# Optimization experiments

Hardware: AMD Instinct MI355X
Metric: run time of the kernel (lower is better)

## Reference

```python
import jax, jax.numpy as jnp
import numpy as np

EPS = 1e-8
LN_EPS = 1e-5
CAPACITY_BETA = 1.5
IDEAL_CLASSES = 5.0

B, F, E, H, C, G = 8192, 1024, 30, 256, 100, 4096


def setup_inputs() -> dict:
    key = jax.random.key(0)
    ks = jax.random.split(key, 8)
    x = jax.random.normal(ks[0], (B, F), dtype=jnp.float32)
    prototypes = jax.random.normal(ks[1], (E, F), dtype=jnp.float32)
    g_new = jax.random.normal(ks[2], (G,), dtype=jnp.float32)
    g_mem = jax.random.normal(ks[3], (E, G), dtype=jnp.float32)
    class_counts = jax.random.randint(ks[4], (E,), 0, 12, dtype=jnp.int32)
    W1 = jax.random.normal(ks[5], (E, F, H), dtype=jnp.float32) * (1.0 / np.sqrt(F))
    b1 = jnp.zeros((E, H), dtype=jnp.float32)
    gamma = jnp.ones((E, H), dtype=jnp.float32)
    beta = jnp.zeros((E, H), dtype=jnp.float32)
    W2 = jax.random.normal(ks[6], (E, H, C), dtype=jnp.float32) * (1.0 / np.sqrt(H))
    b2 = jnp.zeros((E, C), dtype=jnp.float32)
    return {"x": x, "prototypes": prototypes, "g_new": g_new, "g_mem": g_mem,
            "class_counts": class_counts, "W1": W1, "b1": b1, "gamma": gamma,
            "beta": beta, "W2": W2, "b2": b2}


def _route_scores(x, prototypes, g_new, g_mem, class_counts):
    # Cosine similarity of each sample to each expert prototype: [B, E]
    xn = x / (jnp.linalg.norm(x, axis=-1, keepdims=True) + EPS)
    pn = prototypes / (jnp.linalg.norm(prototypes, axis=-1, keepdims=True) + EPS)
    sim = xn @ pn.T
    # Gradient alignment score per expert (cosine of new grad vs EMA memory), mapped to [0, 1]
    gn = g_new / (jnp.linalg.norm(g_new) + EPS)
    gm = g_mem / (jnp.linalg.norm(g_mem, axis=-1, keepdims=True) + EPS)
    align = 0.5 * (1.0 + gm @ gn)  # [E]
    # Capacity penalty: exponential decay once an expert exceeds its ideal class load
    overload = jnp.maximum(class_counts.astype(jnp.float32) / IDEAL_CLASSES - 1.0, 0.0)
    capacity = jnp.exp(-CAPACITY_BETA * overload)  # [E]
    return sim * (align * capacity)[None, :]  # [B, E]


def reference(x, prototypes, g_new, g_mem, class_counts, W1, b1, gamma, beta, W2, b2):
    scores = _route_scores(x, prototypes, g_new, g_mem, class_counts)  # [B, E]
    assign = jnp.argmax(scores, axis=-1)  # [B] expert id per sample
    # Expert MLP: Linear -> LayerNorm -> GELU -> Linear, evaluated for all experts
    h = jnp.einsum('bf,efh->ebh', x, W1) + b1[:, None, :]  # [E, B, H]
    mu = h.mean(axis=-1, keepdims=True)
    var = ((h - mu) ** 2).mean(axis=-1, keepdims=True)
    ln = (h - mu) * jax.lax.rsqrt(var + LN_EPS) * gamma[:, None, :] + beta[:, None, :]
    a = jax.nn.gelu(ln, approximate=False)  # torch nn.GELU default is exact erf
    logits_all = jnp.einsum('ebh,ehc->ebc', a, W2) + b2[:, None, :]  # [E, B, C]
    # Dispatch: each sample keeps only its assigned expert's logits
    logits = logits_all[assign, jnp.arange(x.shape[0])]  # [B, C]
    return logits
```

## Files before the change

### kernel.cpp

```cpp
#include <hip/hip_runtime.h>
#include <hip/hip_bf16.h>
#include <math.h>
#include <float.h>

namespace {
constexpr int Bn = 8192;
constexpr int Fn = 1024;
constexpr int En = 30;
constexpr int Hn = 256;
constexpr int Cn = 100;
constexpr int Gn = 4096;
constexpr int TILECAP64 = 158;
constexpr int TILECAP32 = 285;
constexpr float EPSF  = 1e-8f;
constexpr float LNEPS = 1e-5f;

__device__ __forceinline__ float bf2f(unsigned short u) {
  return __uint_as_float(((unsigned int)u) << 16);
}
__device__ __forceinline__ void unpack8(uint4 u, float* d) {
  unsigned int a[4] = {u.x, u.y, u.z, u.w};
#pragma unroll
  for (int i = 0; i < 4; i++) {
    d[2*i]   = __uint_as_float(a[i] << 16);
    d[2*i+1] = __uint_as_float(a[i] & 0xffff0000u);
  }
}
__device__ __forceinline__ void ld8(const void* base, size_t off, bool f32, float* d) {
  if (f32) {
    const float* p = (const float*)base + off;
    float4 a = *(const float4*)p;
    float4 b = *(const float4*)(p + 4);
    d[0]=a.x; d[1]=a.y; d[2]=a.z; d[3]=a.w;
    d[4]=b.x; d[5]=b.y; d[6]=b.z; d[7]=b.w;
  } else {
    uint4 u = *(const uint4*)((const unsigned short*)base + off);
    unpack8(u, d);
  }
}
__device__ __forceinline__ float ld1(const void* base, size_t off, bool f32) {
  return f32 ? ((const float*)base)[off] : bf2f(((const unsigned short*)base)[off]);
}

typedef _Float16 f16x8 __attribute__((ext_vector_type(8)));
typedef float    f32x4 __attribute__((ext_vector_type(4)));

__device__ __forceinline__ unsigned short f16bits(float v) {
  union { _Float16 f; unsigned short u; } c; c.f = (_Float16)v; return c.u;
}
__device__ __forceinline__ int bswz(int k) { return (k & 7) ^ ((k >> 3) << 2); }
}

#define GLDS16(g, s) __builtin_amdgcn_global_load_lds(                         \
    (const __attribute__((address_space(1))) void*)(uintptr_t)(g),             \
    (__attribute__((address_space(3))) void*)(uintptr_t)(s), 16, 0, 0)

__global__ void k_detect(const unsigned int* __restrict__ gamma_bits,
                         int* __restrict__ flag) {
  if (threadIdx.x == 0) *flag = (gamma_bits[0] == 0x3F800000u) ? 1 : 0;
}

__global__ __launch_bounds__(256) void k_zeroh(float* __restrict__ hbuf) {
  const size_t i = ((size_t)blockIdx.x * 256 + threadIdx.x) * 4;
  *(float4*)(hbuf + i) = make_float4(0.f, 0.f, 0.f, 0.f);
}

__global__ __launch_bounds__(256) void k_route_w(
    const void* __restrict__ protos,
    const void* __restrict__ g_new,
    const void* __restrict__ g_mem,
    const int* __restrict__ ccounts,
    const int* __restrict__ flag,
    float* __restrict__ w) {
  const bool f32 = (*flag != 0);
  const int e = blockIdx.x, t = threadIdx.x;
  float d = 0.f, gm2 = 0.f, gn2 = 0.f, p2 = 0.f;
  for (int g = t; g < Gn; g += 256) {
    float a = ld1(g_new, g, f32);
    float m = ld1(g_mem, (size_t)e * Gn + g, f32);
    d += a * m; gm2 += m * m; gn2 += a * a;
  }
  for (int f = t; f < Fn; f += 256) {
    float v = ld1(protos, (size_t)e * Fn + f, f32);
    p2 += v * v;
  }
#pragma unroll
  for (int m = 1; m < 64; m <<= 1) {
    d   += __shfl_xor(d, m);
    gm2 += __shfl_xor(gm2, m);
    gn2 += __shfl_xor(gn2, m);
    p2  += __shfl_xor(p2, m);
  }
  __shared__ float red[4][4];
  const int lane = t & 63, wid = t >> 6;
  if (lane == 0) { red[wid][0] = d; red[wid][1] = gm2; red[wid][2] = gn2; red[wid][3] = p2; }
  __syncthreads();
  if (t == 0) {
    d   = red[0][0] + red[1][0] + red[2][0] + red[3][0];
    gm2 = red[0][1] + red[1][1] + red[2][1] + red[3][1];
    gn2 = red[0][2] + red[1][2] + red[2][2] + red[3][2];
    p2  = red[0][3] + red[1][3] + red[2][3] + red[3][3];
    float align = 0.5f * (1.0f + d / ((sqrtf(gm2) + EPSF) * (sqrtf(gn2) + EPSF)));
    float over  = fmaxf((float)ccounts[e] / 5.0f - 1.0f, 0.0f);
    float cap   = expf(-1.5f * over);
    w[e] = align * cap / (sqrtf(p2) + EPSF);
  }
}

__global__ __launch_bounds__(256) void k_scores_mfma(
    const float* __restrict__ x,
    const float* __restrict__ protos,
    const float* __restrict__ w,
    const int* __restrict__ flag,
    int* __restrict__ assign) {
  if (*flag == 0) return;
  const int b0 = blockIdx.x * 64;
  extern __shared__ char smem[];
  const int t = threadIdx.x, l = t & 63, wv = t >> 6;

  const char* asrc[4];
#pragma unroll
  for (int i = 0; i < 4; i++) {
    const int D = i * 256 + t, row = D >> 4, pos = D & 15;
    asrc[i] = (const char*)x + (size_t)(b0 + row) * 4096 + (pos ^ (row & 7)) * 16;
  }
  const char* bsrc[2];
#pragma unroll
  for (int i = 0; i < 2; i++) {
    const int D = i * 256 + t, row = D >> 4, pos = D & 15;
    bsrc[i] = (const char*)protos + (size_t)min(row, En - 1) * 4096 +
              (pos ^ (row & 7)) * 16;
  }

  const int r15 = l & 15, kq = l >> 4;
  int addrA[2][2];
#pragma unroll
  for (int ks = 0; ks < 2; ks++)
#pragma unroll
    for (int i = 0; i < 2; i++) {
      const int row = wv * 16 + r15;
      addrA[ks][i] = row * 256 + (((ks * 8 + kq * 2 + i) ^ (row & 7)) * 16);
    }
  int addrB[2][2][2];
#pragma unroll
  for (int nn = 0; nn < 2; nn++)
#pragma unroll
    for (int ks = 0; ks < 2; ks++)
#pragma unroll
      for (int i = 0; i < 2; i++) {
        const int er = nn * 16 + r15;
        addrB[nn][ks][i] = 16384 + er * 256 +
                           (((ks * 8 + kq * 2 + i) ^ (er & 7)) * 16);
      }

  const float w0v = w[r15];
  const float w1v = w[min(r15 + 16, En - 1)];

  f32x4 acc[2];
  acc[0] = (f32x4){0.f, 0.f, 0.f, 0.f};
  acc[1] = (f32x4){0.f, 0.f, 0.f, 0.f};

  auto stage = [&](int buf, int kt) {
    char* bb = smem + buf * 24576;
#pragma unroll
    for (int i = 0; i < 4; i++)
      GLDS16(asrc[i] + kt * 256, bb + i * 4096 + wv * 1024);
#pragma unroll
    for (int i = 0; i < 2; i++)
      GLDS16(bsrc[i] + kt * 256, bb + 16384 + i * 4096 + wv * 1024);
  };

  stage(0, 0);
  __syncthreads();
  int cur = 0;
  for (int kt = 0; kt < 16; ++kt) {
    if (kt < 15) stage(cur ^ 1, kt + 1);
    const char* bb = smem + cur * 24576;
#pragma unroll
    for (int ks = 0; ks < 2; ks++) {
      f16x8 ah, al;
      {
        float4 a0 = *(const float4*)(bb + addrA[ks][0]);
        float4 a1 = *(const float4*)(bb + addrA[ks][1]);
        float av[8] = {a0.x, a0.y, a0.z, a0.w, a1.x, a1.y, a1.z, a1.w};
#pragma unroll
        for (int j = 0; j < 8; j++) {
          _Float16 hh = (_Float16)av[j];
          ah[j] = hh;
          al[j] = (_Float16)(av[j] - (float)hh);
        }
      }
#pragma unroll
      for (int nn = 0; nn < 2; nn++) {
        float4 b0v = *(const float4*)(bb + addrB[nn][ks][0]);
        float4 b1v = *(const float4*)(bb + addrB[nn][ks][1]);
        float bv[8] = {b0v.x, b0v.y, b0v.z, b0v.w, b1v.x, b1v.y, b1v.z, b1v.w};
        f16x8 bh, bl;
#pragma unroll
        for (int j = 0; j < 8; j++) {
          _Float16 hh = (_Float16)bv[j];
          bh[j] = hh;
          bl[j] = (_Float16)(bv[j] - (float)hh);
        }
        acc[nn] = __builtin_amdgcn_mfma_f32_16x16x32_f16(ah, bh, acc[nn], 0, 0, 0);
        acc[nn] = __builtin_amdgcn_mfma_f32_16x16x32_f16(al, bh, acc[nn], 0, 0, 0);
        acc[nn] = __builtin_amdgcn_mfma_f32_16x16x32_f16(ah, bl, acc[nn], 0, 0, 0);
        acc[nn] = __builtin_amdgcn_mfma_f32_16x16x32_f16(al, bl, acc[nn], 0, 0, 0);
      }
    }
    __syncthreads();
    cur ^= 1;
  }

#pragma unroll
  for (int j = 0; j < 4; j++) {
    float best = acc[0][j] * w0v;
    int bi = r15;
    float sc1 = (r15 + 16 < En) ? acc[1][j] * w1v : -FLT_MAX;
    if (sc1 > best) { best = sc1; bi = r15 + 16; }
#pragma unroll
    for (int m = 1; m < 16; m <<= 1) {
      float ov = __shfl_xor(best, m);
      int   oi = __shfl_xor(bi, m);
      if (ov > best || (ov == best && oi < bi)) { best = ov; bi = oi; }
    }
    if (r15 == 0) assign[b0 + wv * 16 + kq * 4 + j] = bi;
  }
}

__global__ __launch_bounds__(256) void k_scores(
    const void* __restrict__ x,
    const void* __restrict__ protos,
    const float* __restrict__ w,
    const int* __restrict__ flag,
    int* __restrict__ assign) {
  const bool f32 = (*flag != 0);
  if (f32) return;
  __shared__ float lx[64][65];
  __shared__ float lp[64][33];
  __shared__ float wl[32];
  __shared__ float redv[64][4];
  __shared__ int   redi[64][4];
  const int t = threadIdx.x;
  const int b0 = blockIdx.x * 64;
  if (t < 32) wl[t] = (t < En) ? w[t] : 0.f;
  const int s = t & 63, eg = t >> 6;
  float acc[8];
#pragma unroll
  for (int j = 0; j < 8; j++) acc[j] = 0.f;

  const int xr = t >> 2, xc = (t & 3) * 16;
  const int pe = t >> 3, pc = (t & 7) * 8;

  for (int kb = 0; kb < Fn; kb += 64) {
    __syncthreads();
    {
      size_t off = (size_t)(b0 + xr) * Fn + kb + xc;
      ld8(x, off,     f32, &lx[xr][xc]);
      ld8(x, off + 8, f32, &lx[xr][xc + 8]);
    }
    if (t < 240) {
      float tmp[8];
      ld8(protos, (size_t)pe * Fn + kb + pc, f32, tmp);
#pragma unroll
      for (int i = 0; i < 8; i++) lp[pc + i][pe] = tmp[i];
    } else {
#pragma unroll
      for (int i = 0; i < 8; i++) { lp[pc + i][30] = 0.f; lp[pc + i][31] = 0.f; }
    }
    __syncthreads();
#pragma unroll 8
    for (int k = 0; k < 64; k++) {
      float xv = lx[s][k];
#pragma unroll
      for (int j = 0; j < 8; j++) acc[j] += xv * lp[k][eg * 8 + j];
    }
  }
  float best = -FLT_MAX; int bi = 0;
#pragma unroll
  for (int j = 0; j < 8; j++) {
    int ee = eg * 8 + j;
    float sc = (ee < En) ? acc[j] * wl[ee] : -FLT_MAX;
    if (sc > best) { best = sc; bi = ee; }
  }
  redv[s][eg] = best; redi[s][eg] = bi;
  __syncthreads();
  if (t < 64) {
    float bv = redv[t][0]; int bx = redi[t][0];
#pragma unroll
    for (int g2 = 1; g2 < 4; g2++) {
      if (redv[t][g2] > bv) { bv = redv[t][g2]; bx = redi[t][g2]; }
    }
    assign[b0 + t] = bx;
  }
}

__global__ void k_zero(int* __restrict__ cnt) {
  if (threadIdx.x < 32) cnt[threadIdx.x] = 0;
}

__global__ void k_bucket(const int* __restrict__ assign,
                         int* __restrict__ cnt,
                         int* __restrict__ list) {
  const int b = blockIdx.x * 256 + threadIdx.x;
  const int e = assign[b];
  const int pos = atomicAdd(&cnt[e], 1);
  list[e * Bn + pos] = b;
}

__global__ void k_plan(const int* __restrict__ cnt,
                       int* __restrict__ tiles64,
                       int* __restrict__ tiles32) {
  if (threadIdx.x == 0) {
    int tot = 0;
    for (int e = 0; e < En; e++) {
      int nt = (cnt[e] + 63) >> 6;
      for (int i = 0; i < nt && tot + i < TILECAP64; i++)
        tiles64[tot + i] = (e << 16) | i;
      tot += nt;
    }
    for (int i = tot; i < TILECAP64; i++) tiles64[i] = -1;
    tot = 0;
    for (int e = 0; e < En; e++) {
      int nt = (cnt[e] + 31) >> 5;
      for (int i = 0; i < nt && tot + i < TILECAP32; i++)
        tiles32[tot + i] = (e << 16) | i;
      tot += nt;
    }
    for (int i = tot; i < TILECAP32; i++) tiles32[i] = -1;
  }
}

__global__ __launch_bounds__(256) void k_l1_f16(
    const float* __restrict__ x,
    const float* __restrict__ W1,
    const float* __restrict__ b1,
    const int* __restrict__ cnt,
    const int* __restrict__ list,
    const int* __restrict__ tiles,
    const int* __restrict__ flag,
    float* __restrict__ hbuf) {
  if (*flag == 0) return;
  const int tv = tiles[blockIdx.x];
  if (tv < 0) return;
  const int e = tv >> 16, ti = tv & 0xffff;
  const int n = cnt[e];
  const int s0 = ti * 64;
  const int ns = min(64, n - s0);
  const int h0 = blockIdx.y * 128;
  const int k0 = blockIdx.z * 16;

  extern __shared__ char smem[];
  __shared__ int idx[64];
  const int t = threadIdx.x, l = t & 63, w = t >> 6;
  if (t < 64) idx[t] = list[e * Bn + s0 + min(t, ns - 1)];
  __syncthreads();

  const char* asrc[2];
#pragma unroll
  for (int i = 0; i < 2; i++) {
    const int D = i * 256 + t, row = D >> 3, pos = D & 7;
    asrc[i] = (const char*)x + (size_t)idx[row] * 4096 + (pos ^ (row & 7)) * 16;
  }
  const char* bsrc[4];
#pragma unroll
  for (int i = 0; i < 4; i++) {
    const int k  = i * 8 + w * 2 + (l >> 5);
    const int c  = (l & 31) ^ bswz(k);
    bsrc[i] = (const char*)W1 +
              ((size_t)(e * Fn + k) * Hn + h0) * 4 + c * 16;
  }

  const int r15 = l & 15, kq = l >> 4;
  int addrA[4][2];
#pragma unroll
  for (int m = 0; m < 4; m++)
#pragma unroll
    for (int i = 0; i < 2; i++) {
      const int row = m * 16 + r15;
      addrA[m][i] = row * 128 + (((kq * 2 + i) ^ (row & 7)) * 16);
    }
  int addrB[2][8];
#pragma unroll
  for (int nn = 0; nn < 2; nn++)
#pragma unroll
    for (int j = 0; j < 8; j++) {
      const int h = w * 32 + nn * 16 + r15;
      const int kl = kq * 8 + j;
      addrB[nn][j] = 8192 + kl * 512 + (((h >> 2) ^ bswz(kl)) * 16) + (h & 3) * 4;
    }

  f32x4 acc[4][2];
#pragma unroll
  for (int m = 0; m < 4; m++)
#pragma unroll
    for (int nn = 0; nn < 2; nn++) acc[m][nn] = (f32x4){0.f, 0.f, 0.f, 0.f};

  auto stage = [&](int buf, int kt) {
    char* bb = smem + buf * 24576;
#pragma unroll
    for (int i = 0; i < 2; i++)
      GLDS16(asrc[i] + kt * 128, bb + i * 4096 + w * 1024);
#pragma unroll
    for (int i = 0; i < 4; i++)
      GLDS16(bsrc[i] + (size_t)kt * 32768, bb + 8192 + i * 4096 + w * 1024);
  };

  stage(0, k0);
  __syncthreads();
  int cur = 0;
  for (int kt = k0; kt < k0 + 16; ++kt) {
    if (kt < k0 + 15) stage(cur ^ 1, kt + 1);
    const char* bb = smem + cur * 24576;

    f16x8 ah[4], al[4];
#pragma unroll
    for (int m = 0; m < 4; m++) {
      float4 a0 = *(const float4*)(bb + addrA[m][0]);
      float4 a1 = *(const float4*)(bb + addrA[m][1]);
      float av[8] = {a0.x, a0.y, a0.z, a0.w, a1.x, a1.y, a1.z, a1.w};
#pragma unroll
      for (int j = 0; j < 8; j++) {
        _Float16 hh = (_Float16)av[j];
        ah[m][j] = hh;
        al[m][j] = (_Float16)(av[j] - (float)hh);
      }
    }
#pragma unroll
    for (int nn = 0; nn < 2; nn++) {
      float bv[8];
#pragma unroll
      for (int j = 0; j < 8; j++)
        bv[j] = *(const float*)(bb + addrB[nn][j]);
      f16x8 bh, bl;
#pragma unroll
      for (int j = 0; j < 8; j++) {
        _Float16 hh = (_Float16)bv[j];
        bh[j] = hh;
        bl[j] = (_Float16)(bv[j] - (float)hh);
      }
#pragma unroll
      for (int m = 0; m < 4; m++) {
        acc[m][nn] = __builtin_amdgcn_mfma_f32_16x16x32_f16(ah[m], bh, acc[m][nn], 0, 0, 0);
        acc[m][nn] = __builtin_amdgcn_mfma_f32_16x16x32_f16(al[m], bh, acc[m][nn], 0, 0, 0);
        acc[m][nn] = __builtin_amdgcn_mfma_f32_16x16x32_f16(ah[m], bl, acc[m][nn], 0, 0, 0);
      }
    }
    __syncthreads();
    cur ^= 1;
  }

  float bias[2];
#pragma unroll
  for (int nn = 0; nn < 2; nn++)
    bias[nn] = (blockIdx.z == 0)
             ? b1[(size_t)e * Hn + h0 + w * 32 + nn * 16 + r15] : 0.f;
#pragma unroll
  for (int m = 0; m < 4; m++) {
#pragma unroll
    for (int j = 0; j < 4; j++) {
      const int r = m * 16 + kq * 4 + j;
      if (r < ns) {
        float* dst = hbuf + (size_t)idx[r] * Hn + h0 + w * 32;
#pragma unroll
        for (int nn = 0; nn < 2; nn++)
          atomicAdd(dst + nn * 16 + r15, acc[m][nn][j] + bias[nn]);
      }
    }
  }
}

__global__ __launch_bounds__(256) void k_layer1_valu(
    const void* __restrict__ x,
    const void* __restrict__ W1,
    const void* __restrict__ b1,
    const int* __restrict__ cnt,
    const int* __restrict__ list,
    const int* __restrict__ flag,
    float* __restrict__ hbuf) {
  if (*flag != 0) return;
  const int e = blockIdx.x;
  const int n = cnt[e];
  const int s0 = blockIdx.y * 64;
  if (s0 >= n) return;
  const int ns = min(64, n - s0);
  const int h0 = blockIdx.z * 64;
  const int t = threadIdx.x;

  __shared__ int   idx[64];
  __shared__ float lx[64][33];
  __shared__ float lw[32][68];

  if (t < 64) idx[t] = list[e * Bn + s0 + min(t, ns - 1)];
  __syncthreads();

  const int hg = t & 15;
  const int sg = t >> 4;
  float acc[4][4];
#pragma unroll
  for (int i = 0; i < 4; i++)
#pragma unroll
    for (int j = 0; j < 4; j++) acc[i][j] = 0.f;

  const int xr = t >> 2, xc = (t & 3) * 8;
  const int wk = t >> 3, wc = (t & 7) * 8;

  for (int kb = 0; kb < Fn; kb += 32) {
    ld8(x, (size_t)idx[xr] * Fn + kb + xc, false, &lx[xr][xc]);
    ld8(W1, ((size_t)e * Fn + kb + wk) * Hn + h0 + wc, false, &lw[wk][wc]);
    __syncthreads();
#pragma unroll
    for (int k = 0; k < 32; k++) {
      float xv[4], wv[4];
#pragma unroll
      for (int i = 0; i < 4; i++) xv[i] = lx[sg * 4 + i][k];
#pragma unroll
      for (int j = 0; j < 4; j++) wv[j] = lw[k][hg * 4 + j];
#pragma unroll
      for (int i = 0; i < 4; i++)
#pragma unroll
        for (int j = 0; j < 4; j++) acc[i][j] = fmaf(xv[i], wv[j], acc[i][j]);
    }
    __syncthreads();
  }
  float bias[4];
#pragma unroll
  for (int j = 0; j < 4; j++) bias[j] = ld1(b1, (size_t)e * Hn + h0 + hg * 4 + j, false);
#pragma unroll
  for (int i = 0; i < 4; i++) {
    int srow = sg * 4 + i;
    if (srow < ns) {
      float4 v = make_float4(acc[i][0] + bias[0], acc[i][1] + bias[1],
                             acc[i][2] + bias[2], acc[i][3] + bias[3]);
      *(float4*)(&hbuf[(size_t)idx[srow] * Hn + h0 + hg * 4]) = v;
    }
  }
}

__global__ __launch_bounds__(256) void k_ln2_mfma(
    const float* __restrict__ hbuf,
    const float* __restrict__ gamma,
    const float* __restrict__ beta,
    const float* __restrict__ W2,
    const float* __restrict__ b2,
    const int* __restrict__ cnt,
    const int* __restrict__ list,
    const int* __restrict__ tiles32,
    const int* __restrict__ flag,
    float* __restrict__ out) {
  if (*flag == 0) return;
  const int tv = tiles32[blockIdx.x];
  if (tv < 0) return;
  const int e = tv >> 16, ti = tv & 0xffff;
  const int n = cnt[e];
  const int s0 = ti * 32;
  const int ns = min(32, n - s0);

  __shared__ __align__(16) char aT[32 * 1024];
  __shared__ __align__(16) char bW[2][13312];
  __shared__ int idx[32];

  const int t = threadIdx.x, l = t & 63, w = t >> 6;
  if (t < 32) idx[t] = list[e * Bn + s0 + min(t, ns - 1)];

  const char* w2e = (const char*)W2 + (size_t)e * (Hn * Cn * 4);
  auto stageB = [&](int buf, int kt) {
    const int base = kt * 12800;
    for (int i = w; i < 13; i += 4) {
      int off = base + i * 1024 + l * 16;
      if (off > 102400 - 16) off = 102400 - 16;
      GLDS16(w2e + off, bW[buf] + i * 1024);
    }
  };

  stageB(0, 0);
  __syncthreads();

  const int s = t >> 3, seg = t & 7;
  const int b = idx[s];
  float hv[32];
  float sum = 0.f, sq = 0.f;
  {
    const float* src = hbuf + (size_t)b * Hn + seg * 32;
#pragma unroll
    for (int i = 0; i < 32; i += 4) {
      float4 v = *(const float4*)(src + i);
      hv[i] = v.x; hv[i+1] = v.y; hv[i+2] = v.z; hv[i+3] = v.w;
      sum += v.x + v.y + v.z + v.w;
      sq  += v.x*v.x + v.y*v.y + v.z*v.z + v.w*v.w;
    }
  }
#pragma unroll
  for (int m = 1; m < 8; m <<= 1) { sum += __shfl_xor(sum, m); sq += __shfl_xor(sq, m); }
  const float mu = sum * (1.f / 256.f);
  float var = fmaxf(sq * (1.f / 256.f) - mu * mu, 0.f);
  const float rstd = rsqrtf(var + LNEPS);
#pragma unroll
  for (int i4 = 0; i4 < 8; i4++) {
    float av[4];
#pragma unroll
    for (int j = 0; j < 4; j++) {
      const int hh = seg * 32 + i4 * 4 + j;
      const float g  = gamma[(size_t)e * Hn + hh];
      const float be = beta[(size_t)e * Hn + hh];
      const float ln = (hv[i4 * 4 + j] - mu) * rstd * g + be;
      av[j] = 0.5f * ln * (1.0f + erff(ln * 0.70710678118654752f));
    }
    const int chunk = (seg * 8 + i4) ^ (s & 7);
    *(float4*)(aT + s * 1024 + chunk * 16) = make_float4(av[0], av[1], av[2], av[3]);
  }

  const int r15 = l & 15, kq = l >> 4;
  int addrB[2][8];
#pragma unroll
  for (int ni = 0; ni < 2; ni++) {
    const int nt = w + ni * 4;
    const int c = nt * 16 + r15;
#pragma unroll
    for (int j = 0; j < 8; j++)
      addrB[ni][j] = ((kq * 8 + j) * Cn + c) * 4;
  }

  f32x4 acc[2][2];
#pragma unroll
  for (int m = 0; m < 2; m++)
#pragma unroll
    for (int ni = 0; ni < 2; ni++) acc[m][ni] = (f32x4){0.f, 0.f, 0.f, 0.f};

  __syncthreads();

  int cur = 0;
  for (int kt = 0; kt < 8; ++kt) {
    if (kt < 7) stageB(cur ^ 1, kt + 1);

    f16x8 ah[2], al[2];
#pragma unroll
    for (int m = 0; m < 2; m++) {
      const int row = m * 16 + r15;
      const int c0 = (kt * 8 + kq * 2) ^ (row & 7);
      const int c1 = (kt * 8 + kq * 2 + 1) ^ (row & 7);
      float4 a0 = *(const float4*)(aT + row * 1024 + c0 * 16);
      float4 a1 = *(const float4*)(aT + row * 1024 + c1 * 16);
      float av[8] = {a0.x, a0.y, a0.z, a0.w, a1.x, a1.y, a1.z, a1.w};
#pragma unroll
      for (int j = 0; j < 8; j++) {
        _Float16 hh = (_Float16)av[j];
        ah[m][j] = hh;
        al[m][j] = (_Float16)(av[j] - (float)hh);
      }
    }
#pragma unroll
    for (int ni = 0; ni < 2; ni++) {
      const int nt = w + ni * 4;
      if (nt < 7) {
        float bv[8];
#pragma unroll
        for (int j = 0; j < 8; j++)
          bv[j] = *(const float*)(bW[cur] + addrB[ni][j]);
        f16x8 bh, bl;
#pragma unroll
        for (int j = 0; j < 8; j++) {
          _Float16 hh = (_Float16)bv[j];
          bh[j] = hh;
          bl[j] = (_Float16)(bv[j] - (float)hh);
        }
#pragma unroll
        for (int m = 0; m < 2; m++) {
          acc[m][ni] = __builtin_amdgcn_mfma_f32_16x16x32_f16(ah[m], bh, acc[m][ni], 0, 0, 0);
          acc[m][ni] = __builtin_amdgcn_mfma_f32_16x16x32_f16(al[m], bh, acc[m][ni], 0, 0, 0);
          acc[m][ni] = __builtin_amdgcn_mfma_f32_16x16x32_f16(ah[m], bl, acc[m][ni], 0, 0, 0);
        }
      }
    }
    __syncthreads();
    cur ^= 1;
  }

#pragma unroll
  for (int ni = 0; ni < 2; ni++) {
    const int nt = w + ni * 4;
    if (nt >= 7) continue;
    const int c = nt * 16 + r15;
    if (c >= Cn) continue;
    const float bias = b2[(size_t)e * Cn + c];
#pragma unroll
    for (int m = 0; m < 2; m++) {
#pragma unroll
      for (int j = 0; j < 4; j++) {
        const int r = m * 16 + kq * 4 + j;
        if (r < ns)
          out[(size_t)idx[r] * Cn + c] = acc[m][ni][j] + bias;
      }
    }
  }
}

__global__ __launch_bounds__(256) void k_ln_l2(
    const float* __restrict__ hbuf,
    const void* __restrict__ gamma,
    const void* __restrict__ beta,
    const void* __restrict__ W2,
    const void* __restrict__ b2,
    const int* __restrict__ cnt,
    const int* __restrict__ list,
    const int* __restrict__ flag,
    void* __restrict__ out) {
  const bool f32 = (*flag != 0);
  if (f32) return;
  const int e = blockIdx.x;
  const int n = cnt[e];
  const int s0 = blockIdx.y * 32;
  if (s0 >= n) return;
  const int ns = min(32, n - s0);
  const int t = threadIdx.x;

  __shared__ int   idx[32];
  __shared__ float a_lds[32][257];
  __shared__ float lw2[64][104];

  if (t < 32) idx[t] = list[e * Bn + s0 + min(t, ns - 1)];
  __syncthreads();

  const int s = t >> 3;
  const int seg = t & 7;
  const int b = idx[s];

  float hv[32];
  float sum = 0.f, sq = 0.f;
  {
    const float* src = hbuf + (size_t)b * Hn + seg * 32;
#pragma unroll
    for (int i = 0; i < 32; i += 4) {
      float4 v = *(const float4*)(src + i);
      hv[i] = v.x; hv[i+1] = v.y; hv[i+2] = v.z; hv[i+3] = v.w;
      sum += v.x + v.y + v.z + v.w;
      sq  += v.x*v.x + v.y*v.y + v.z*v.z + v.w*v.w;
    }
  }
#pragma unroll
  for (int m = 1; m < 8; m <<= 1) { sum += __shfl_xor(sum, m); sq += __shfl_xor(sq, m); }
  const float mu = sum * (1.f / 256.f);
  float var = sq * (1.f / 256.f) - mu * mu;
  var = fmaxf(var, 0.f);
  const float rstd = rsqrtf(var + LNEPS);
#pragma unroll
  for (int i = 0; i < 32; i++) {
    int hh = seg * 32 + i;
    float g  = ld1(gamma, (size_t)e * Hn + hh, f32);
    float be = ld1(beta,  (size_t)e * Hn + hh, f32);
    float ln = (hv[i] - mu) * rstd * g + be;
    float aa = 0.5f * ln * (1.0f + erff(ln * 0.70710678118654752f));
    a_lds[s][hh] = aa;
  }

  const int cg = t & 7;
  const int so = t >> 3;
  float acc[13];
#pragma unroll
  for (int j = 0; j < 13; j++) acc[j] = 0.f;

  for (int hb = 0; hb < Hn; hb += 64) {
    __syncthreads();
    for (int u = t; u < 64 * 104; u += 256) {
      int k = u / 104;
      int c = u - k * 104;
      lw2[k][c] = (c < Cn) ? ld1(W2, ((size_t)e * Hn + hb + k) * Cn + c, f32) : 0.f;
    }
    __syncthreads();
#pragma unroll 8
    for (int h = 0; h < 64; h++) {
      float av = a_lds[so][hb + h];
#pragma unroll
      for (int j = 0; j < 13; j++) acc[j] += av * lw2[h][cg + 8 * j];
    }
  }
  if (so < ns) {
    int bb = idx[so];
#pragma unroll
    for (int j = 0; j < 13; j++) {
      int c = cg + 8 * j;
      if (c < Cn) {
        float v = acc[j] + ld1(b2, (size_t)e * Cn + c, f32);
        ((__hip_bfloat16*)out)[(size_t)bb * Cn + c] = __float2bfloat16(v);
      }
    }
  }
}

extern "C" void kernel_launch(void* const* d_in, const int* in_sizes, int n_in,
                              void* d_out, int out_size, void* d_ws, size_t ws_size,
                              hipStream_t stream) {
  const void* x       = d_in[0];
  const void* protos  = d_in[1];
  const void* g_new   = d_in[2];
  const void* g_mem   = d_in[3];
  const int*  ccounts = (const int*)d_in[4];
  const void* W1      = d_in[5];
  const void* b1      = d_in[6];
  const void* gamma   = d_in[7];
  const void* beta    = d_in[8];
  const void* W2      = d_in[9];
  const void* b2      = d_in[10];

  char* ws = (char*)d_ws;
  float* w       = (float*)(ws);
  int*   flag    = (int*)(ws + 384);
  int*   assign  = (int*)(ws + 512);
  int*   tiles64 = (int*)(ws + 512);
  int*   tiles32 = (int*)(ws + 512 + 1024);
  int*   cnt     = (int*)(ws + 512 + Bn * 4);
  int*   list    = (int*)(ws + 512 + Bn * 4 + 256);
  float* hbuf    = (float*)(ws + 1016576);

  k_detect<<<1, 64, 0, stream>>>((const unsigned int*)gamma, flag);
  k_route_w<<<dim3(En), 256, 0, stream>>>(protos, g_new, g_mem, ccounts, flag, w);
  k_scores_mfma<<<dim3(Bn / 64), 256, 49152, stream>>>(
      (const float*)x, (const float*)protos, w, flag, assign);
  k_scores<<<dim3(Bn / 64), 256, 0, stream>>>(x, protos, w, flag, assign);
  k_zero<<<1, 64, 0, stream>>>(cnt);
  k_bucket<<<Bn / 256, 256, 0, stream>>>(assign, cnt, list);
  k_plan<<<1, 64, 0, stream>>>(cnt, tiles64, tiles32);
  k_zeroh<<<dim3((Bn * Hn) / (256 * 4)), 256, 0, stream>>>(hbuf);
  k_l1_f16<<<dim3(TILECAP64, 2, 2), 256, 49152, stream>>>(
      (const float*)x, (const float*)W1, (const float*)b1,
      cnt, list, tiles64, flag, hbuf);
  k_layer1_valu<<<dim3(En, 128, 4), 256, 0, stream>>>(
      x, W1, b1, cnt, list, flag, hbuf);
  k_ln2_mfma<<<dim3(TILECAP32), 256, 0, stream>>>(
      hbuf, (const float*)gamma, (const float*)beta, (const float*)W2,
      (const float*)b2, cnt, list, tiles32, flag, (float*)d_out);
  k_ln_l2<<<dim3(En, 256), 256, 0, stream>>>(
      hbuf, gamma, beta, W2, b2, cnt, list, flag, d_out);
}
```

Baseline: 258.5 us.

## Drop bf16 fallback path, fuse small launches, and retile score and layer-1 grids

Removes the runtime dtype-detect kernel and all bf16 fallback kernels, which in the fp32 case launched and then exited early. Folds the count zeroing into the routing-weight kernel and the tile planning into the hidden-buffer zeroing kernel, cutting the launch count. The score kernel now uses 32-row blocks, with each wave handling one 16-row by 16-expert tile and an LDS merge across the two expert halves. Layer 1 now splits K four ways instead of two, giving more blocks at the cost of more atomics. The code now assumes fp32 inputs only.

```diff
diff --git a/kernel.cpp b/kernel.cpp
--- a/kernel.cpp
+++ b/kernel.cpp
@@ -15,39 +15,9 @@
 constexpr float EPSF  = 1e-8f;
 constexpr float LNEPS = 1e-5f;
 
-__device__ __forceinline__ float bf2f(unsigned short u) {
-  return __uint_as_float(((unsigned int)u) << 16);
-}
-__device__ __forceinline__ void unpack8(uint4 u, float* d) {
-  unsigned int a[4] = {u.x, u.y, u.z, u.w};
-#pragma unroll
-  for (int i = 0; i < 4; i++) {
-    d[2*i]   = __uint_as_float(a[i] << 16);
-    d[2*i+1] = __uint_as_float(a[i] & 0xffff0000u);
-  }
-}
-__device__ __forceinline__ void ld8(const void* base, size_t off, bool f32, float* d) {
-  if (f32) {
-    const float* p = (const float*)base + off;
-    float4 a = *(const float4*)p;
-    float4 b = *(const float4*)(p + 4);
-    d[0]=a.x; d[1]=a.y; d[2]=a.z; d[3]=a.w;
-    d[4]=b.x; d[5]=b.y; d[6]=b.z; d[7]=b.w;
-  } else {
-    uint4 u = *(const uint4*)((const unsigned short*)base + off);
-    unpack8(u, d);
-  }
-}
-__device__ __forceinline__ float ld1(const void* base, size_t off, bool f32) {
-  return f32 ? ((const float*)base)[off] : bf2f(((const unsigned short*)base)[off]);
-}
-
 typedef _Float16 f16x8 __attribute__((ext_vector_type(8)));
 typedef float    f32x4 __attribute__((ext_vector_type(4)));
 
-__device__ __forceinline__ unsigned short f16bits(float v) {
-  union { _Float16 f; unsigned short u; } c; c.f = (_Float16)v; return c.u;
-}
 __device__ __forceinline__ int bswz(int k) { return (k & 7) ^ ((k >> 3) << 2); }
 }
 
@@ -55,33 +25,23 @@
     (const __attribute__((address_space(1))) void*)(uintptr_t)(g),             \
     (__attribute__((address_space(3))) void*)(uintptr_t)(s), 16, 0, 0)
 
-__global__ void k_detect(const unsigned int* __restrict__ gamma_bits,
-                         int* __restrict__ flag) {
-  if (threadIdx.x == 0) *flag = (gamma_bits[0] == 0x3F800000u) ? 1 : 0;
-}
-
-__global__ __launch_bounds__(256) void k_zeroh(float* __restrict__ hbuf) {
-  const size_t i = ((size_t)blockIdx.x * 256 + threadIdx.x) * 4;
-  *(float4*)(hbuf + i) = make_float4(0.f, 0.f, 0.f, 0.f);
-}
-
 __global__ __launch_bounds__(256) void k_route_w(
-    const void* __restrict__ protos,
-    const void* __restrict__ g_new,
-    const void* __restrict__ g_mem,
+    const float* __restrict__ protos,
+    const float* __restrict__ g_new,
+    const float* __restrict__ g_mem,
     const int* __restrict__ ccounts,
-    const int* __restrict__ flag,
-    float* __restrict__ w) {
-  const bool f32 = (*flag != 0);
+    float* __restrict__ w,
+    int* __restrict__ cnt) {
   const int e = blockIdx.x, t = threadIdx.x;
+  if (e == 0 && t < 32) cnt[t] = 0;
   float d = 0.f, gm2 = 0.f, gn2 = 0.f, p2 = 0.f;
   for (int g = t; g < Gn; g += 256) {
-    float a = ld1(g_new, g, f32);
-    float m = ld1(g_mem, (size_t)e * Gn + g, f32);
+    float a = g_new[g];
+    float m = g_mem[(size_t)e * Gn + g];
     d += a * m; gm2 += m * m; gn2 += a * a;
   }
   for (int f = t; f < Fn; f += 256) {
-    float v = ld1(protos, (size_t)e * Fn + f, f32);
+    float v = protos[(size_t)e * Fn + f];
     p2 += v * v;
   }
 #pragma unroll
@@ -111,16 +71,17 @@
     const float* __restrict__ x,
     const float* __restrict__ protos,
     const float* __restrict__ w,
-    const int* __restrict__ flag,
     int* __restrict__ assign) {
-  if (*flag == 0) return;
-  const int b0 = blockIdx.x * 64;
+  const int b0 = blockIdx.x * 32;
   extern __shared__ char smem[];
+  __shared__ float av_[32][2];
+  __shared__ int   ai_[32][2];
   const int t = threadIdx.x, l = t & 63, wv = t >> 6;
-
-  const char* asrc[4];
-#pragma unroll
-  for (int i = 0; i < 4; i++) {
+  const int mt = wv >> 1, nt = wv & 1;
+
+  const char* asrc[2];
+#pragma unroll
+  for (int i = 0; i < 2; i++) {
     const int D = i * 256 + t, row = D >> 4, pos = D & 15;
     asrc[i] = (const char*)x + (size_t)(b0 + row) * 4096 + (pos ^ (row & 7)) * 16;
   }
@@ -138,36 +99,32 @@
   for (int ks = 0; ks < 2; ks++)
 #pragma unroll
     for (int i = 0; i < 2; i++) {
-      const int row = wv * 16 + r15;
+      const int row = mt * 16 + r15;
       addrA[ks][i] = row * 256 + (((ks * 8 + kq * 2 + i) ^ (row & 7)) * 16);
     }
-  int addrB[2][2][2];
-#pragma unroll
-  for (int nn = 0; nn < 2; nn++)
-#pragma unroll
-    for (int ks = 0; ks < 2; ks++)
-#pragma unroll
-      for (int i = 0; i < 2; i++) {
-        const int er = nn * 16 + r15;
-        addrB[nn][ks][i] = 16384 + er * 256 +
-                           (((ks * 8 + kq * 2 + i) ^ (er & 7)) * 16);
-      }
-
-  const float w0v = w[r15];
-  const float w1v = w[min(r15 + 16, En - 1)];
-
-  f32x4 acc[2];
-  acc[0] = (f32x4){0.f, 0.f, 0.f, 0.f};
-  acc[1] = (f32x4){0.f, 0.f, 0.f, 0.f};
+  int addrB[2][2];
+#pragma unroll
+  for (int ks = 0; ks < 2; ks++)
+#pragma unroll
+    for (int i = 0; i < 2; i++) {
+      const int er = nt * 16 + r15;
+      addrB[ks][i] = 8192 + er * 256 + (((ks * 8 + kq * 2 + i) ^ (er & 7)) * 16);
+    }
+
+  const int  e_w   = nt * 16 + r15;
+  const bool valid = (e_w < En);
+  const float wsc  = w[min(e_w, En - 1)];
+
+  f32x4 acc = (f32x4){0.f, 0.f, 0.f, 0.f};
 
   auto stage = [&](int buf, int kt) {
-    char* bb = smem + buf * 24576;
-#pragma unroll
-    for (int i = 0; i < 4; i++)
+    char* bb = smem + buf * 16384;
+#pragma unroll
+    for (int i = 0; i < 2; i++)
       GLDS16(asrc[i] + kt * 256, bb + i * 4096 + wv * 1024);
 #pragma unroll
     for (int i = 0; i < 2; i++)
-      GLDS16(bsrc[i] + kt * 256, bb + 16384 + i * 4096 + wv * 1024);
+      GLDS16(bsrc[i] + kt * 256, bb + 8192 + i * 4096 + wv * 1024);
   };
 
   stage(0, 0);
@@ -175,7 +132,7 @@
   int cur = 0;
   for (int kt = 0; kt < 16; ++kt) {
     if (kt < 15) stage(cur ^ 1, kt + 1);
-    const char* bb = smem + cur * 24576;
+    const char* bb = smem + cur * 16384;
 #pragma unroll
     for (int ks = 0; ks < 2; ks++) {
       f16x8 ah, al;
@@ -190,23 +147,22 @@
           al[j] = (_Float16)(av[j] - (float)hh);
         }
       }
-#pragma unroll
-      for (int nn = 0; nn < 2; nn++) {
-        float4 b0v = *(const float4*)(bb + addrB[nn][ks][0]);
-        float4 b1v = *(const float4*)(bb + addrB[nn][ks][1]);
+      f16x8 bh, bl;
+      {
+        float4 b0v = *(const float4*)(bb + addrB[ks][0]);
+        float4 b1v = *(const float4*)(bb + addrB[ks][1]);
         float bv[8] = {b0v.x, b0v.y, b0v.z, b0v.w, b1v.x, b1v.y, b1v.z, b1v.w};
-        f16x8 bh, bl;
 #pragma unroll
         for (int j = 0; j < 8; j++) {
           _Float16 hh = (_Float16)bv[j];
           bh[j] = hh;
           bl[j] = (_Float16)(bv[j] - (float)hh);
         }
-        acc[nn] = __builtin_amdgcn_mfma_f32_16x16x32_f16(ah, bh, acc[nn], 0, 0, 0);
-        acc[nn] = __builtin_amdgcn_mfma_f32_16x16x32_f16(al, bh, acc[nn], 0, 0, 0);
-        acc[nn] = __builtin_amdgcn_mfma_f32_16x16x32_f16(ah, bl, acc[nn], 0, 0, 0);
-        acc[nn] = __builtin_amdgcn_mfma_f32_16x16x32_f16(al, bl, acc[nn], 0, 0, 0);
-      }
+      }
+      acc = __builtin_amdgcn_mfma_f32_16x16x32_f16(ah, bh, acc, 0, 0, 0);
+      acc = __builtin_amdgcn_mfma_f32_16x16x32_f16(al, bh, acc, 0, 0, 0);
+      acc = __builtin_amdgcn_mfma_f32_16x16x32_f16(ah, bl, acc, 0, 0, 0);
+      acc = __builtin_amdgcn_mfma_f32_16x16x32_f16(al, bl, acc, 0, 0, 0);
     }
     __syncthreads();
     cur ^= 1;
@@ -214,89 +170,25 @@
 
 #pragma unroll
   for (int j = 0; j < 4; j++) {
-    float best = acc[0][j] * w0v;
-    int bi = r15;
-    float sc1 = (r15 + 16 < En) ? acc[1][j] * w1v : -FLT_MAX;
-    if (sc1 > best) { best = sc1; bi = r15 + 16; }
+    float best = valid ? acc[j] * wsc : -FLT_MAX;
+    int bi = e_w;
 #pragma unroll
     for (int m = 1; m < 16; m <<= 1) {
       float ov = __shfl_xor(best, m);
       int   oi = __shfl_xor(bi, m);
       if (ov > best || (ov == best && oi < bi)) { best = ov; bi = oi; }
     }
-    if (r15 == 0) assign[b0 + wv * 16 + kq * 4 + j] = bi;
-  }
-}
-
-__global__ __launch_bounds__(256) void k_scores(
-    const void* __restrict__ x,
-    const void* __restrict__ protos,
-    const float* __restrict__ w,
-    const int* __restrict__ flag,
-    int* __restrict__ assign) {
-  const bool f32 = (*flag != 0);
-  if (f32) return;
-  __shared__ float lx[64][65];
-  __shared__ float lp[64][33];
-  __shared__ float wl[32];
-  __shared__ float redv[64][4];
-  __shared__ int   redi[64][4];
-  const int t = threadIdx.x;
-  const int b0 = blockIdx.x * 64;
-  if (t < 32) wl[t] = (t < En) ? w[t] : 0.f;
-  const int s = t & 63, eg = t >> 6;
-  float acc[8];
-#pragma unroll
-  for (int j = 0; j < 8; j++) acc[j] = 0.f;
-
-  const int xr = t >> 2, xc = (t & 3) * 16;
-  const int pe = t >> 3, pc = (t & 7) * 8;
-
-  for (int kb = 0; kb < Fn; kb += 64) {
-    __syncthreads();
-    {
-      size_t off = (size_t)(b0 + xr) * Fn + kb + xc;
-      ld8(x, off,     f32, &lx[xr][xc]);
-      ld8(x, off + 8, f32, &lx[xr][xc + 8]);
-    }
-    if (t < 240) {
-      float tmp[8];
-      ld8(protos, (size_t)pe * Fn + kb + pc, f32, tmp);
-#pragma unroll
-      for (int i = 0; i < 8; i++) lp[pc + i][pe] = tmp[i];
-    } else {
-#pragma unroll
-      for (int i = 0; i < 8; i++) { lp[pc + i][30] = 0.f; lp[pc + i][31] = 0.f; }
-    }
-    __syncthreads();
-#pragma unroll 8
-    for (int k = 0; k < 64; k++) {
-      float xv = lx[s][k];
-#pragma unroll
-      for (int j = 0; j < 8; j++) acc[j] += xv * lp[k][eg * 8 + j];
-    }
-  }
-  float best = -FLT_MAX; int bi = 0;
-#pragma unroll
-  for (int j = 0; j < 8; j++) {
-    int ee = eg * 8 + j;
-    float sc = (ee < En) ? acc[j] * wl[ee] : -FLT_MAX;
-    if (sc > best) { best = sc; bi = ee; }
-  }
-  redv[s][eg] = best; redi[s][eg] = bi;
-  __syncthreads();
-  if (t < 64) {
-    float bv = redv[t][0]; int bx = redi[t][0];
-#pragma unroll
-    for (int g2 = 1; g2 < 4; g2++) {
-      if (redv[t][g2] > bv) { bv = redv[t][g2]; bx = redi[t][g2]; }
-    }
-    assign[b0 + t] = bx;
-  }
-}
-
-__global__ void k_zero(int* __restrict__ cnt) {
-  if (threadIdx.x < 32) cnt[threadIdx.x] = 0;
+    if (r15 == 0) {
+      const int s = mt * 16 + kq * 4 + j;
+      av_[s][nt] = best;
+      ai_[s][nt] = bi;
+    }
+  }
+  __syncthreads();
+  if (t < 32) {
+    const float v0 = av_[t][0], v1 = av_[t][1];
+    assign[b0 + t] = (v1 > v0) ? ai_[t][1] : ai_[t][0];
+  }
 }
 
 __global__ void k_bucket(const int* __restrict__ assign,
@@ -308,26 +200,30 @@
   list[e * Bn + pos] = b;
 }
 
-__global__ void k_plan(const int* __restrict__ cnt,
-                       int* __restrict__ tiles64,
-                       int* __restrict__ tiles32) {
-  if (threadIdx.x == 0) {
+__global__ __launch_bounds__(256) void k_planz(
+    const int* __restrict__ cnt,
+    int* __restrict__ tiles64,
+    int* __restrict__ tiles32,
+    float* __restrict__ hbuf) {
+  const size_t i = ((size_t)blockIdx.x * 256 + threadIdx.x) * 4;
+  *(float4*)(hbuf + i) = make_float4(0.f, 0.f, 0.f, 0.f);
+  if (blockIdx.x == 0 && threadIdx.x == 0) {
     int tot = 0;
     for (int e = 0; e < En; e++) {
       int nt = (cnt[e] + 63) >> 6;
-      for (int i = 0; i < nt && tot + i < TILECAP64; i++)
-        tiles64[tot + i] = (e << 16) | i;
+      for (int k = 0; k < nt && tot + k < TILECAP64; k++)
+        tiles64[tot + k] = (e << 16) | k;
       tot += nt;
     }
-    for (int i = tot; i < TILECAP64; i++) tiles64[i] = -1;
+    for (int k = tot; k < TILECAP64; k++) tiles64[k] = -1;
     tot = 0;
     for (int e = 0; e < En; e++) {
       int nt = (cnt[e] + 31) >> 5;
-      for (int i = 0; i < nt && tot + i < TILECAP32; i++)
-        tiles32[tot + i] = (e << 16) | i;
+      for (int k = 0; k < nt && tot + k < TILECAP32; k++)
+        tiles32[tot + k] = (e << 16) | k;
       tot += nt;
     }
-    for (int i = tot; i < TILECAP32; i++) tiles32[i] = -1;
+    for (int k = tot; k < TILECAP32; k++) tiles32[k] = -1;
   }
 }
 
@@ -338,9 +234,7 @@
     const int* __restrict__ cnt,
     const int* __restrict__ list,
     const int* __restrict__ tiles,
-    const int* __restrict__ flag,
     float* __restrict__ hbuf) {
-  if (*flag == 0) return;
   const int tv = tiles[blockIdx.x];
   if (tv < 0) return;
   const int e = tv >> 16, ti = tv & 0xffff;
@@ -348,7 +242,7 @@
   const int s0 = ti * 64;
   const int ns = min(64, n - s0);
   const int h0 = blockIdx.y * 128;
-  const int k0 = blockIdx.z * 16;
+  const int k0 = blockIdx.z * 8;
 
   extern __shared__ char smem[];
   __shared__ int idx[64];
@@ -409,8 +303,8 @@
   stage(0, k0);
   __syncthreads();
   int cur = 0;
-  for (int kt = k0; kt < k0 + 16; ++kt) {
-    if (kt < k0 + 15) stage(cur ^ 1, kt + 1);
+  for (int kt = k0; kt < k0 + 8; ++kt) {
+    if (kt < k0 + 7) stage(cur ^ 1, kt + 1);
     const char* bb = smem + cur * 24576;
 
     f16x8 ah[4], al[4];
@@ -466,73 +360,6 @@
         for (int nn = 0; nn < 2; nn++)
           atomicAdd(dst + nn * 16 + r15, acc[m][nn][j] + bias[nn]);
       }
-    }
-  }
-}
-
-__global__ __launch_bounds__(256) void k_layer1_valu(
-    const void* __restrict__ x,
-    const void* __restrict__ W1,
-    const void* __restrict__ b1,
-    const int* __restrict__ cnt,
-    const int* __restrict__ list,
-    const int* __restrict__ flag,
-    float* __restrict__ hbuf) {
-  if (*flag != 0) return;
-  const int e = blockIdx.x;
-  const int n = cnt[e];
-  const int s0 = blockIdx.y * 64;
-  if (s0 >= n) return;
-  const int ns = min(64, n - s0);
-  const int h0 = blockIdx.z * 64;
-  const int t = threadIdx.x;
-
-  __shared__ int   idx[64];
-  __shared__ float lx[64][33];
-  __shared__ float lw[32][68];
-
-  if (t < 64) idx[t] = list[e * Bn + s0 + min(t, ns - 1)];
-  __syncthreads();
-
-  const int hg = t & 15;
-  const int sg = t >> 4;
-  float acc[4][4];
-#pragma unroll
-  for (int i = 0; i < 4; i++)
-#pragma unroll
-    for (int j = 0; j < 4; j++) acc[i][j] = 0.f;
-
-  const int xr = t >> 2, xc = (t & 3) * 8;
-  const int wk = t >> 3, wc = (t & 7) * 8;
-
-  for (int kb = 0; kb < Fn; kb += 32) {
-    ld8(x, (size_t)idx[xr] * Fn + kb + xc, false, &lx[xr][xc]);
-    ld8(W1, ((size_t)e * Fn + kb + wk) * Hn + h0 + wc, false, &lw[wk][wc]);
-    __syncthreads();
-#pragma unroll
-    for (int k = 0; k < 32; k++) {
-      float xv[4], wv[4];
-#pragma unroll
-      for (int i = 0; i < 4; i++) xv[i] = lx[sg * 4 + i][k];
-#pragma unroll
-      for (int j = 0; j < 4; j++) wv[j] = lw[k][hg * 4 + j];
-#pragma unroll
-      for (int i = 0; i < 4; i++)
-#pragma unroll
-        for (int j = 0; j < 4; j++) acc[i][j] = fmaf(xv[i], wv[j], acc[i][j]);
-    }
-    __syncthreads();
-  }
-  float bias[4];
-#pragma unroll
-  for (int j = 0; j < 4; j++) bias[j] = ld1(b1, (size_t)e * Hn + h0 + hg * 4 + j, false);
-#pragma unroll
-  for (int i = 0; i < 4; i++) {
-    int srow = sg * 4 + i;
-    if (srow < ns) {
-      float4 v = make_float4(acc[i][0] + bias[0], acc[i][1] + bias[1],
-                             acc[i][2] + bias[2], acc[i][3] + bias[3]);
-      *(float4*)(&hbuf[(size_t)idx[srow] * Hn + h0 + hg * 4]) = v;
     }
   }
 }
@@ -546,9 +373,7 @@
     const int* __restrict__ cnt,
     const int* __restrict__ list,
     const int* __restrict__ tiles32,
-    const int* __restrict__ flag,
     float* __restrict__ out) {
-  if (*flag == 0) return;
   const int tv = tiles32[blockIdx.x];
   if (tv < 0) return;
   const int e = tv >> 16, ti = tv & 0xffff;
@@ -690,98 +515,6 @@
         const int r = m * 16 + kq * 4 + j;
         if (r < ns)
           out[(size_t)idx[r] * Cn + c] = acc[m][ni][j] + bias;
-      }
-    }
-  }
-}
-
-__global__ __launch_bounds__(256) void k_ln_l2(
-    const float* __restrict__ hbuf,
-    const void* __restrict__ gamma,
-    const void* __restrict__ beta,
-    const void* __restrict__ W2,
-    const void* __restrict__ b2,
-    const int* __restrict__ cnt,
-    const int* __restrict__ list,
-    const int* __restrict__ flag,
-    void* __restrict__ out) {
-  const bool f32 = (*flag != 0);
-  if (f32) return;
-  const int e = blockIdx.x;
-  const int n = cnt[e];
-  const int s0 = blockIdx.y * 32;
-  if (s0 >= n) return;
-  const int ns = min(32, n - s0);
-  const int t = threadIdx.x;
-
-  __shared__ int   idx[32];
-  __shared__ float a_lds[32][257];
-  __shared__ float lw2[64][104];
-
-  if (t < 32) idx[t] = list[e * Bn + s0 + min(t, ns - 1)];
-  __syncthreads();
-
-  const int s = t >> 3;
-  const int seg = t & 7;
-  const int b = idx[s];
-
-  float hv[32];
-  float sum = 0.f, sq = 0.f;
-  {
-    const float* src = hbuf + (size_t)b * Hn + seg * 32;
-#pragma unroll
-    for (int i = 0; i < 32; i += 4) {
-      float4 v = *(const float4*)(src + i);
-      hv[i] = v.x; hv[i+1] = v.y; hv[i+2] = v.z; hv[i+3] = v.w;
-      sum += v.x + v.y + v.z + v.w;
-      sq  += v.x*v.x + v.y*v.y + v.z*v.z + v.w*v.w;
-    }
-  }
-#pragma unroll
-  for (int m = 1; m < 8; m <<= 1) { sum += __shfl_xor(sum, m); sq += __shfl_xor(sq, m); }
-  const float mu = sum * (1.f / 256.f);
-  float var = sq * (1.f / 256.f) - mu * mu;
-  var = fmaxf(var, 0.f);
-  const float rstd = rsqrtf(var + LNEPS);
-#pragma unroll
-  for (int i = 0; i < 32; i++) {
-    int hh = seg * 32 + i;
-    float g  = ld1(gamma, (size_t)e * Hn + hh, f32);
-    float be = ld1(beta,  (size_t)e * Hn + hh, f32);
-    float ln = (hv[i] - mu) * rstd * g + be;
-    float aa = 0.5f * ln * (1.0f + erff(ln * 0.70710678118654752f));
-    a_lds[s][hh] = aa;
-  }
-
-  const int cg = t & 7;
-  const int so = t >> 3;
-  float acc[13];
-#pragma unroll
-  for (int j = 0; j < 13; j++) acc[j] = 0.f;
-
-  for (int hb = 0; hb < Hn; hb += 64) {
-    __syncthreads();
-    for (int u = t; u < 64 * 104; u += 256) {
-      int k = u / 104;
-      int c = u - k * 104;
-      lw2[k][c] = (c < Cn) ? ld1(W2, ((size_t)e * Hn + hb + k) * Cn + c, f32) : 0.f;
-    }
-    __syncthreads();
-#pragma unroll 8
-    for (int h = 0; h < 64; h++) {
-      float av = a_lds[so][hb + h];
-#pragma unroll
-      for (int j = 0; j < 13; j++) acc[j] += av * lw2[h][cg + 8 * j];
-    }
-  }
-  if (so < ns) {
-    int bb = idx[so];
-#pragma unroll
-    for (int j = 0; j < 13; j++) {
-      int c = cg + 8 * j;
-      if (c < Cn) {
-        float v = acc[j] + ld1(b2, (size_t)e * Cn + c, f32);
-        ((__hip_bfloat16*)out)[(size_t)bb * Cn + c] = __float2bfloat16(v);
       }
     }
   }
@@ -801,10 +534,10 @@
   const void* beta    = d_in[8];
   const void* W2      = d_in[9];
   const void* b2      = d_in[10];
+  (void)gamma; (void)beta;
 
   char* ws = (char*)d_ws;
   float* w       = (float*)(ws);
-  int*   flag    = (int*)(ws + 384);
   int*   assign  = (int*)(ws + 512);
   int*   tiles64 = (int*)(ws + 512);
   int*   tiles32 = (int*)(ws + 512 + 1024);
@@ -812,23 +545,18 @@
   int*   list    = (int*)(ws + 512 + Bn * 4 + 256);
   float* hbuf    = (float*)(ws + 1016576);
 
-  k_detect<<<1, 64, 0, stream>>>((const unsigned int*)gamma, flag);
-  k_route_w<<<dim3(En), 256, 0, stream>>>(protos, g_new, g_mem, ccounts, flag, w);
-  k_scores_mfma<<<dim3(Bn / 64), 256, 49152, stream>>>(
-      (const float*)x, (const float*)protos, w, flag, assign);
-  k_scores<<<dim3(Bn / 64), 256, 0, stream>>>(x, protos, w, flag, assign);
-  k_zero<<<1, 64, 0, stream>>>(cnt);
+  k_route_w<<<dim3(En), 256, 0, stream>>>(
+      (const float*)protos, (const float*)g_new, (const float*)g_mem,
+      ccounts, w, cnt);
+  k_scores_mfma<<<dim3(Bn / 32), 256, 32768, stream>>>(
+      (const float*)x, (const float*)protos, w, assign);
   k_bucket<<<Bn / 256, 256, 0, stream>>>(assign, cnt, list);
-  k_plan<<<1, 64, 0, stream>>>(cnt, tiles64, tiles32);
-  k_zeroh<<<dim3((Bn * Hn) / (256 * 4)), 256, 0, stream>>>(hbuf);
-  k_l1_f16<<<dim3(TILECAP64, 2, 2), 256, 49152, stream>>>(
+  k_planz<<<dim3((Bn * Hn) / (256 * 4)), 256, 0, stream>>>(
+      cnt, tiles64, tiles32, hbuf);
+  k_l1_f16<<<dim3(TILECAP64, 2, 4), 256, 49152, stream>>>(
       (const float*)x, (const float*)W1, (const float*)b1,
-      cnt, list, tiles64, flag, hbuf);
-  k_layer1_valu<<<dim3(En, 128, 4), 256, 0, stream>>>(
-      x, W1, b1, cnt, list, flag, hbuf);
+      cnt, list, tiles64, hbuf);
   k_ln2_mfma<<<dim3(TILECAP32), 256, 0, stream>>>(
       hbuf, (const float*)gamma, (const float*)beta, (const float*)W2,
-      (const float*)b2, cnt, list, tiles32, flag, (float*)d_out);
-  k_ln_l2<<<dim3(En, 256), 256, 0, stream>>>(
-      hbuf, gamma, beta, W2, b2, cnt, list, flag, d_out);
-}
+      (const float*)b2, cnt, list, tiles32, (float*)d_out);
+}
```

Measured after the change: 242.8 us. 1.06x faster.
